# Optimization experiments

Hardware: AMD Instinct MI355X
Metric: run time of the kernel (lower is better)

## Reference

```python
import jax, jax.numpy as jnp
import numpy as np

N_NODES = 100000
N_EDGES = 300000
N_GRAPHS = 4096
EMB = 256
L = 5
EPS = 1e-5


def setup_inputs() -> dict:
    key = jax.random.key(0)
    ks = jax.random.split(key, 16)
    x = jax.random.normal(ks[0], (N_NODES, 40), dtype=jnp.float32)
    edge_index = jax.random.randint(ks[1], (2, N_EDGES), 0, N_NODES, dtype=jnp.int32)
    edge_attr = jax.random.normal(ks[2], (N_EDGES, 10), dtype=jnp.float32)
    batch = jnp.sort(jax.random.randint(ks[3], (N_NODES,), 0, N_GRAPHS, dtype=jnp.int32))
    s = lambda fan: 1.0 / np.sqrt(fan)
    params = {
        "x_emb_W": jax.random.normal(ks[4], (EMB, 40), jnp.float32) * np.sqrt(2.0 / 40),
        "x_emb_b": jnp.zeros((EMB,), jnp.float32),
        "e_emb_W": jax.random.normal(ks[5], (EMB, 10), jnp.float32) * np.sqrt(2.0 / 10),
        "e_emb_b": jnp.zeros((EMB,), jnp.float32),
        "gcn_W": jax.random.normal(ks[6], (L, EMB, EMB), jnp.float32) * s(EMB),
        "gcn_b": jax.random.normal(ks[7], (L, EMB), jnp.float32) * s(EMB),
        "root_emb": jax.random.normal(ks[8], (L, EMB), jnp.float32),
        "bn_gamma": jnp.ones((L, EMB), jnp.float32),
        "bn_beta": jnp.zeros((L, EMB), jnp.float32),
        "p1_W": jax.random.normal(ks[9], (EMB // 2, EMB), jnp.float32) * s(EMB),
        "p1_b": jnp.zeros((EMB // 2,), jnp.float32),
        "p2_W": jax.random.normal(ks[10], (EMB // 2, EMB // 2), jnp.float32) * s(EMB // 2),
        "p2_b": jnp.zeros((EMB // 2,), jnp.float32),
        "p3_W": jax.random.normal(ks[11], (1, EMB // 2), jnp.float32) * s(EMB // 2),
        "p3_b": jnp.zeros((1,), jnp.float32),
    }
    return dict(x=x, edge_index=edge_index, edge_attr=edge_attr, batch=batch, **params)


def _gcn_conv(h, row, col, ea, W, b, root):
    # h: [N, D] node feats; ea: [E, D] edge feats
    hx = h @ W.T + b
    deg = jax.ops.segment_sum(jnp.ones_like(row, dtype=hx.dtype), row, num_segments=N_NODES) + 1.0
    dinv = deg ** -0.5
    norm = dinv[row] * dinv[col]                      # [E]
    msg = norm[:, None] * jax.nn.relu(hx[row] + ea)   # gather + relu + scale
    agg = jax.ops.segment_sum(msg, col, num_segments=N_NODES)  # scatter-add to targets
    return agg + jax.nn.relu(hx + root) / deg[:, None]


def _batchnorm(h, gamma, beta):
    mean = jnp.mean(h, axis=0)
    var = jnp.var(h, axis=0)
    return (h - mean) * jax.lax.rsqrt(var + EPS) * gamma + beta


def reference(x, edge_index, edge_attr, batch,
              x_emb_W, x_emb_b, e_emb_W, e_emb_b,
              gcn_W, gcn_b, root_emb, bn_gamma, bn_beta,
              p1_W, p1_b, p2_W, p2_b, p3_W, p3_b):
    row, col = edge_index[0], edge_index[1]
    h = x @ x_emb_W.T + x_emb_b
    ea = edge_attr @ e_emb_W.T + e_emb_b
    for l in range(L):
        h_in = h
        h = _gcn_conv(h, row, col, ea, gcn_W[l], gcn_b[l], root_emb[l])
        h = _batchnorm(h_in + h, bn_gamma[l], bn_beta[l])
        if l != L - 1:
            h = jax.nn.relu(h)
        # dropout is identity in eval mode
    # global mean pool over graphs
    sums = jax.ops.segment_sum(h, batch, num_segments=N_GRAPHS)
    cnts = jax.ops.segment_sum(jnp.ones((h.shape[0],), h.dtype), batch, num_segments=N_GRAPHS)
    g = sums / jnp.maximum(cnts, 1.0)[:, None]
    # prediction head: Lin-ReLU-Lin-ReLU-Lin
    g = jax.nn.relu(g @ p1_W.T + p1_b)
    g = jax.nn.relu(g @ p2_W.T + p2_b)
    return g @ p3_W.T + p3_b
```

## Files before the change

kernel.cpp:

```cpp
#include <hip/hip_runtime.h>
#include <hip/hip_bf16.h>

#define NN 100000
#define NE 300000
#define NG 4096
#define EMB 256
#define NLAYERS 5

typedef unsigned short u16;
typedef unsigned int u32;

typedef short bf16x8 __attribute__((ext_vector_type(8)));
typedef float f32x4 __attribute__((ext_vector_type(4)));

__device__ __forceinline__ float b2f(u16 u){
    union { float f; u32 i; } v; v.i = ((u32)u) << 16; return v.f;
}
__device__ __forceinline__ u16 f2b(float f){
    __hip_bfloat16 h = __float2bfloat16(f);
    union { __hip_bfloat16 h; u16 u; } v; v.h = h; return v.u;
}

#define XNB 32
__global__ __launch_bounds__(256) void embed_x(const float* __restrict__ x,
        const float* __restrict__ W, const float* __restrict__ b,
        u16* __restrict__ t)
{
    __shared__ float sW[256][41];
    __shared__ float sx[XNB][40];
    int tid = threadIdx.x;
    for (int i = tid; i < 256*40; i += 256) sW[i/40][i%40] = W[i];
    int n0 = blockIdx.x * XNB;
    for (int i = tid; i < XNB*40; i += 256) {
        int j = i/40, k = i%40;
        sx[j][k] = x[(size_t)(n0+j)*40 + k];
    }
    __syncthreads();
    float bb = b[tid];
    for (int j = 0; j < XNB; ++j) {
        float a = bb;
        #pragma unroll
        for (int k = 0; k < 40; ++k) a = fmaf(sW[tid][k], sx[j][k], a);
        t[(size_t)(n0+j)*EMB + tid] = f2b(a);
    }
}

__global__ void wconv(const float* __restrict__ W, u16* __restrict__ Wb, int n)
{
    int i = blockIdx.x*256 + threadIdx.x;
    if (i < n) Wb[i] = f2b(W[i]);
}

__global__ void ewt_kernel(const float* __restrict__ eW, float* __restrict__ eWt)
{
    int i = blockIdx.x*256 + threadIdx.x;
    if (i < 2560) { int f = i/10, k = i%10; eWt[k*256 + f] = eW[i]; }
}

__global__ void hist_kernel(const int* __restrict__ row, const int* __restrict__ col,
        int* __restrict__ rcnt, int* __restrict__ ccnt, int E)
{
    int e = blockIdx.x*256 + threadIdx.x;
    if (e < E) {
        atomicAdd(&rcnt[row[e]], 1);
        atomicAdd(&ccnt[col[e]], 1);
    }
}

__global__ void deg_fin(const int* __restrict__ rcnt, float* __restrict__ dinv,
                        float* __restrict__ invdg, int N)
{
    int n = blockIdx.x*256 + threadIdx.x;
    if (n < N) {
        float d = (float)rcnt[n] + 1.0f;
        dinv[n]  = rsqrtf(d);
        invdg[n] = 1.0f/d;
    }
}

__global__ void scan1(const int* __restrict__ cnt, int* __restrict__ bsum, int N)
{
    __shared__ int sh[256];
    int t = threadIdx.x, i = blockIdx.x*256 + t;
    sh[t] = (i < N) ? cnt[i] : 0;
    __syncthreads();
    for (int off = 128; off > 0; off >>= 1) {
        if (t < off) sh[t] += sh[t+off];
        __syncthreads();
    }
    if (t == 0) bsum[blockIdx.x] = sh[0];
}

__global__ __launch_bounds__(512) void scan2(const int* __restrict__ bsum,
        int* __restrict__ bbase, int* __restrict__ coff, int nb)
{
    __shared__ int a[512], b[512];
    int t = threadIdx.x;
    a[t] = (t < nb) ? bsum[t] : 0;
    __syncthreads();
    int* src = a; int* dst = b;
    for (int off = 1; off < 512; off <<= 1) {
        dst[t] = (t >= off) ? src[t-off] + src[t] : src[t];
        __syncthreads();
        int* tmp = src; src = dst; dst = tmp;
    }
    bbase[t] = t ? src[t-1] : 0;
    if (t == 0) coff[NN] = NE;
}

__global__ void scan3(const int* __restrict__ cnt, const int* __restrict__ bbase,
        int* __restrict__ coff, int N)
{
    __shared__ int a[256], b[256];
    int t = threadIdx.x, i = blockIdx.x*256 + t;
    a[t] = (i < N) ? cnt[i] : 0;
    __syncthreads();
    int* src = a; int* dst = b;
    for (int off = 1; off < 256; off <<= 1) {
        dst[t] = (t >= off) ? src[t-off] + src[t] : src[t];
        __syncthreads();
        int* tmp = src; src = dst; dst = tmp;
    }
    if (i < N) coff[i] = bbase[blockIdx.x] + (t ? src[t-1] : 0);
}

__global__ void csr_fill(const int* __restrict__ row, const int* __restrict__ col,
        const float* __restrict__ eattr, const int* __restrict__ coff,
        const float* __restrict__ dinv, int* __restrict__ fill,
        int* __restrict__ erow, float* __restrict__ enorm,
        u16* __restrict__ eab, int E)
{
    int e = blockIdx.x*256 + threadIdx.x;
    if (e < E) {
        int c = col[e], r = row[e];
        int p = coff[c] + atomicAdd(&fill[c], 1);
        erow[p]  = r;
        enorm[p] = dinv[r] * dinv[c];
        #pragma unroll
        for (int k = 0; k < 10; ++k) eab[(size_t)p*16 + k] = f2b(eattr[(size_t)e*10 + k]);
        #pragma unroll
        for (int k = 10; k < 16; ++k) eab[(size_t)p*16 + k] = 0;
    }
}

__global__ __launch_bounds__(512) void gemm_mfma(const u16* __restrict__ A,
        const u16* __restrict__ Wb, const float* __restrict__ bias,
        const float* __restrict__ bnsc, int doBN,
        u16* __restrict__ C, int M)
{
    __shared__ u16 As[128*64];
    __shared__ u16 Bs[256*64];
    __shared__ float scS[256], shS[256];
    const int tid = threadIdx.x;
    if (doBN && tid < 256) { scS[tid] = bnsc[tid]; shS[tid] = bnsc[256+tid]; }
    const int wid  = tid >> 6;
    const int lane = tid & 63;
    const int wm = wid >> 2, wn = wid & 3;
    const int m0 = blockIdx.x * 128;
    __syncthreads();
    f32x4 acc[4][4] = {};
    for (int k0 = 0; k0 < 256; k0 += 64) {
        #pragma unroll
        for (int i = 0; i < 2; ++i) {
            int L = tid + i*512;
            int rowi = L >> 3, ch = L & 7;
            int sw = ch ^ (rowi & 7);
            int gr = m0 + rowi; gr = gr < M ? gr : M-1;
            uint4 va = *reinterpret_cast<const uint4*>(&A[(size_t)gr*256 + k0 + ch*8]);
            if (doBN) {
                int kk = k0 + ch*8;
                u32 wv[4] = {va.x, va.y, va.z, va.w};
                #pragma unroll
                for (int j = 0; j < 4; ++j) {
                    float lo = b2f((u16)(wv[j] & 0xffffu));
                    float hi = b2f((u16)(wv[j] >> 16));
                    lo = fmaxf(fmaf(lo, scS[kk+2*j],   shS[kk+2*j]),   0.f);
                    hi = fmaxf(fmaf(hi, scS[kk+2*j+1], shS[kk+2*j+1]), 0.f);
                    wv[j] = (u32)f2b(lo) | ((u32)f2b(hi) << 16);
                }
                va.x = wv[0]; va.y = wv[1]; va.z = wv[2]; va.w = wv[3];
            }
            *reinterpret_cast<uint4*>(&As[(rowi*8 + sw)*8]) = va;
        }
        #pragma unroll
        for (int i = 0; i < 4; ++i) {
            int L = tid + i*512;
            int rowi = L >> 3, ch = L & 7;
            int sw = ch ^ (rowi & 7);
            uint4 vb = *reinterpret_cast<const uint4*>(&Wb[(size_t)rowi*256 + k0 + ch*8]);
            *reinterpret_cast<uint4*>(&Bs[(rowi*8 + sw)*8]) = vb;
        }
        __syncthreads();
        const int c = lane >> 4;
        const int rl = lane & 15;
        #pragma unroll
        for (int kt = 0; kt < 2; ++kt) {
            bf16x8 af[4], bfr[4];
            #pragma unroll
            for (int f = 0; f < 4; ++f) {
                int ra = wm*64 + f*16 + rl;
                int cha = (kt*4 + c) ^ (ra & 7);
                af[f] = *reinterpret_cast<const bf16x8*>(&As[(ra*8 + cha)*8]);
                int rb = wn*64 + f*16 + rl;
                int chb = (kt*4 + c) ^ (rb & 7);
                bfr[f] = *reinterpret_cast<const bf16x8*>(&Bs[(rb*8 + chb)*8]);
            }
            #pragma unroll
            for (int fm = 0; fm < 4; ++fm)
                #pragma unroll
                for (int fn = 0; fn < 4; ++fn)
                    acc[fm][fn] = __builtin_amdgcn_mfma_f32_16x16x32_bf16(
                        af[fm], bfr[fn], acc[fm][fn], 0, 0, 0);
        }
        __syncthreads();
    }
    const int cn = lane & 15, rq = lane >> 4;
    #pragma unroll
    for (int fn = 0; fn < 4; ++fn) {
        int n = wn*64 + fn*16 + cn;
        float bb = bias[n];
        #pragma unroll
        for (int fm = 0; fm < 4; ++fm) {
            #pragma unroll
            for (int r = 0; r < 4; ++r) {
                int m = m0 + wm*64 + fm*16 + rq*4 + r;
                if (m < M) C[(size_t)m*256 + n] = f2b(acc[fm][fn][r] + bb);
            }
        }
    }
}

#define GFB 4
#define NGROUPS (NN/GFB)
__global__ __launch_bounds__(256) void gather_combine(const int* __restrict__ erow,
        const float* __restrict__ enorm, const u16* __restrict__ eab,
        const int* __restrict__ coff,
        const float* __restrict__ eWt, const float* __restrict__ ebv,
        const u16* __restrict__ hx, const float* __restrict__ rootv,
        const float* __restrict__ invdg, const float* __restrict__ bnscPrev,
        int doBN, u16* __restrict__ t, float* __restrict__ stats, int N)
{
    __shared__ float red[4][512];
    const int wid = threadIdx.x >> 6, lane = threadIdx.x & 63;
    const int f4 = lane*4;
    float w[4][10], bb[4];
    #pragma unroll
    for (int k = 0; k < 10; ++k) {
        float4 wv = *reinterpret_cast<const float4*>(&eWt[k*256 + f4]);
        w[0][k] = wv.x; w[1][k] = wv.y; w[2][k] = wv.z; w[3][k] = wv.w;
    }
    { float4 bv = *reinterpret_cast<const float4*>(&ebv[f4]);
      bb[0]=bv.x; bb[1]=bv.y; bb[2]=bv.z; bb[3]=bv.w; }
    float4 root = *reinterpret_cast<const float4*>(&rootv[f4]);
    float sc[4] = {1,1,1,1}, sh[4] = {0,0,0,0};
    if (doBN) {
        float4 s = *reinterpret_cast<const float4*>(&bnscPrev[f4]);
        float4 b = *reinterpret_cast<const float4*>(&bnscPrev[256+f4]);
        sc[0]=s.x; sc[1]=s.y; sc[2]=s.z; sc[3]=s.w;
        sh[0]=b.x; sh[1]=b.y; sh[2]=b.z; sh[3]=b.w;
    }
    float sacc[4] = {0,0,0,0}, s2acc[4] = {0,0,0,0};

    for (int g = blockIdx.x*4 + wid; g < NGROUPS; g += gridDim.x*4) {
        const int nb = g*GFB;
        int c1 = coff[nb+1], c2 = coff[nb+2], c3 = coff[nb+3], c4 = coff[nb+4];
        int s = coff[nb], e = c4;
        int jn = 0, cend = c1;
        float acc[4] = {0,0,0,0};

        #define FLUSH() do {                                                   \
            int n_ = nb + jn;                                                  \
            size_t idx_ = (size_t)n_*EMB + f4;                                 \
            uint2 hv_ = *reinterpret_cast<const uint2*>(&t[idx_]);             \
            uint2 xv_ = *reinterpret_cast<const uint2*>(&hx[idx_]);            \
            float id_ = invdg[n_];                                             \
            float hh_[4] = { b2f((u16)(hv_.x&0xffffu)), b2f((u16)(hv_.x>>16)), \
                             b2f((u16)(hv_.y&0xffffu)), b2f((u16)(hv_.y>>16)) };\
            float xx_[4] = { b2f((u16)(xv_.x&0xffffu)), b2f((u16)(xv_.x>>16)), \
                             b2f((u16)(xv_.y&0xffffu)), b2f((u16)(xv_.y>>16)) };\
            float rt_[4] = { root.x, root.y, root.z, root.w };                 \
            u16 ov_[4];                                                        \
            _Pragma("unroll")                                                  \
            for (int jj = 0; jj < 4; ++jj) {                                   \
                float hin_ = hh_[jj];                                          \
                if (doBN) hin_ = fmaxf(fmaf(hin_, sc[jj], sh[jj]), 0.f);       \
                float rv_ = xx_[jj] + rt_[jj];                                 \
                rv_ = rv_ > 0.f ? rv_ : 0.f;                                   \
                float tv_ = hin_ + acc[jj] + rv_*id_;                          \
                ov_[jj] = f2b(tv_);                                            \
                sacc[jj] += tv_; s2acc[jj] += tv_*tv_;                         \
                acc[jj] = 0.f;                                                 \
            }                                                                  \
            uint2 o_; o_.x = (u32)ov_[0] | ((u32)ov_[1]<<16);                  \
            o_.y = (u32)ov_[2] | ((u32)ov_[3]<<16);                            \
            *reinterpret_cast<uint2*>(&t[idx_]) = o_;                          \
            ++jn; cend = (jn==1) ? c2 : (jn==2) ? c3 : c4;                     \
        } while(0)

        #define CONSUME(nm, hvv, alo, ahi) do {                                \
            float hf_[4] = { b2f((u16)((hvv).x&0xffffu)), b2f((u16)((hvv).x>>16)),\
                             b2f((u16)((hvv).y&0xffffu)), b2f((u16)((hvv).y>>16)) };\
            float at_[10];                                                     \
            at_[0]=b2f((u16)((alo).x&0xffffu)); at_[1]=b2f((u16)((alo).x>>16));\
            at_[2]=b2f((u16)((alo).y&0xffffu)); at_[3]=b2f((u16)((alo).y>>16));\
            at_[4]=b2f((u16)((alo).z&0xffffu)); at_[5]=b2f((u16)((alo).z>>16));\
            at_[6]=b2f((u16)((alo).w&0xffffu)); at_[7]=b2f((u16)((alo).w>>16));\
            at_[8]=b2f((u16)((ahi).x&0xffffu)); at_[9]=b2f((u16)((ahi).x>>16));\
            _Pragma("unroll")                                                  \
            for (int jj = 0; jj < 4; ++jj) {                                   \
                float ea_ = bb[jj];                                            \
                _Pragma("unroll")                                              \
                for (int k = 0; k < 10; ++k) ea_ = fmaf(at_[k], w[jj][k], ea_);\
                float v_ = hf_[jj] + ea_;                                      \
                acc[jj] += v_ > 0.f ? v_*(nm) : 0.f;                           \
            }                                                                  \
        } while(0)

        int p = s;
        for (; p + 4 <= e; p += 4) {
            int r0 = erow[p], r1 = erow[p+1], r2 = erow[p+2], r3 = erow[p+3];
            float n0 = enorm[p], n1 = enorm[p+1], n2 = enorm[p+2], n3 = enorm[p+3];
            uint2 h0 = *reinterpret_cast<const uint2*>(&hx[(size_t)r0*EMB + f4]);
            uint2 h1 = *reinterpret_cast<const uint2*>(&hx[(size_t)r1*EMB + f4]);
            uint2 h2 = *reinterpret_cast<const uint2*>(&hx[(size_t)r2*EMB + f4]);
            uint2 h3 = *reinterpret_cast<const uint2*>(&hx[(size_t)r3*EMB + f4]);
            uint4 a0l = *reinterpret_cast<const uint4*>(&eab[(size_t)(p+0)*16]);
            uint4 a0h = *reinterpret_cast<const uint4*>(&eab[(size_t)(p+0)*16+8]);
            uint4 a1l = *reinterpret_cast<const uint4*>(&eab[(size_t)(p+1)*16]);
            uint4 a1h = *reinterpret_cast<const uint4*>(&eab[(size_t)(p+1)*16+8]);
            uint4 a2l = *reinterpret_cast<const uint4*>(&eab[(size_t)(p+2)*16]);
            uint4 a2h = *reinterpret_cast<const uint4*>(&eab[(size_t)(p+2)*16+8]);
            uint4 a3l = *reinterpret_cast<const uint4*>(&eab[(size_t)(p+3)*16]);
            uint4 a3h = *reinterpret_cast<const uint4*>(&eab[(size_t)(p+3)*16+8]);
            while (p+0 >= cend) FLUSH();
            CONSUME(n0, h0, a0l, a0h);
            while (p+1 >= cend) FLUSH();
            CONSUME(n1, h1, a1l, a1h);
            while (p+2 >= cend) FLUSH();
            CONSUME(n2, h2, a2l, a2h);
            while (p+3 >= cend) FLUSH();
            CONSUME(n3, h3, a3l, a3h);
        }
        for (; p < e; ++p) {
            int r0 = erow[p];
            float n0 = enorm[p];
            uint2 h0 = *reinterpret_cast<const uint2*>(&hx[(size_t)r0*EMB + f4]);
            uint4 a0l = *reinterpret_cast<const uint4*>(&eab[(size_t)p*16]);
            uint4 a0h = *reinterpret_cast<const uint4*>(&eab[(size_t)p*16+8]);
            while (p >= cend) FLUSH();
            CONSUME(n0, h0, a0l, a0h);
        }
        while (jn < GFB) FLUSH();
        #undef FLUSH
        #undef CONSUME
    }

    #pragma unroll
    for (int j = 0; j < 4; ++j) {
        red[wid][f4+j]     = sacc[j];
        red[wid][256+f4+j] = s2acc[j];
    }
    __syncthreads();
    int tt = threadIdx.x;
    float a0 = red[0][tt] + red[1][tt] + red[2][tt] + red[3][tt];
    float a1 = red[0][256+tt] + red[1][256+tt] + red[2][256+tt] + red[3][256+tt];
    atomicAdd(&stats[tt], a0);
    atomicAdd(&stats[256+tt], a1);
}

__global__ void bn_finalize(const float* __restrict__ stats,
        const float* __restrict__ gamma, const float* __restrict__ beta,
        float* __restrict__ sc, int N)
{
    int f = threadIdx.x;
    float inv = 1.0f / (float)N;
    float mean = stats[f] * inv;
    float var  = stats[256+f] * inv - mean*mean;
    float is = rsqrtf(var + 1e-5f);
    float scale = gamma[f] * is;
    sc[f] = scale;
    sc[256+f] = fmaf(-mean, scale, beta[f]);
}

__global__ __launch_bounds__(256) void pool_kernel(const u16* __restrict__ t,
        const int* __restrict__ batch, const float* __restrict__ bnsc4,
        float* __restrict__ psum, float* __restrict__ pcnt, int N)
{
    int tid = threadIdx.x;
    int half = tid >> 7;
    int pp = tid & 127;
    const u32* t32 = (const u32*)t;
    float sc0 = bnsc4[2*pp],     sc1 = bnsc4[2*pp+1];
    float sh0 = bnsc4[256+2*pp], sh1 = bnsc4[256+2*pp+1];
    int n0 = blockIdx.x * 256;
    int n1 = min(n0 + 256, N);
    int start = n0 + half;
    if (start >= n1) return;
    int cur = batch[start];
    float a0 = 0.f, a1 = 0.f;
    int cnt = 0;
    for (int n = start; n < n1; n += 2) {
        int gb = batch[n];
        if (gb != cur) {
            atomicAdd(&psum[(size_t)cur*EMB + 2*pp],   a0);
            atomicAdd(&psum[(size_t)cur*EMB + 2*pp+1], a1);
            if (pp == 0) atomicAdd(&pcnt[cur], (float)cnt);
            a0 = a1 = 0.f; cnt = 0; cur = gb;
        }
        u32 v = t32[(size_t)n*128 + pp];
        a0 += fmaf(b2f((u16)(v & 0xffffu)), sc0, sh0);
        a1 += fmaf(b2f((u16)(v >> 16)),     sc1, sh1);
        ++cnt;
    }
    atomicAdd(&psum[(size_t)cur*EMB + 2*pp],   a0);
    atomicAdd(&psum[(size_t)cur*EMB + 2*pp+1], a1);
    if (pp == 0) atomicAdd(&pcnt[cur], (float)cnt);
}

__global__ void pool2g(const float* __restrict__ psum, const float* __restrict__ pcnt,
        u16* __restrict__ gbf)
{
    int i = blockIdx.x*256 + threadIdx.x;
    if (i < NG*128) {
        int g = i >> 7, p2 = (i & 127)*2;
        float invc = 1.0f / fmaxf(pcnt[g], 1.0f);
        u32 pk = (u32)f2b(psum[(size_t)g*EMB + p2] * invc)
               | ((u32)f2b(psum[(size_t)g*EMB + p2 + 1] * invc) << 16);
        ((u32*)gbf)[i] = pk;
    }
}

__global__ __launch_bounds__(256) void gemm_head(const u16* __restrict__ A,
        const u16* __restrict__ W, const float* __restrict__ bias,
// ... 42 lines not shown
                        af[fm], bfr[fn], acc[fm][fn], 0, 0, 0);
        }
        __syncthreads();
    }
    const int cn = lane & 15, rq = lane >> 4;
    #pragma unroll
    for (int fn = 0; fn < 4; ++fn) {
        int n = wc*64 + fn*16 + cn;
        float bb = bias[n];
        #pragma unroll
        for (int fm = 0; fm < 4; ++fm) {
            #pragma unroll
            for (int r = 0; r < 4; ++r) {
                int m = m0 + wr*64 + fm*16 + rq*4 + r;
                if (m < M) C[(size_t)m*128 + n] = f2b(fmaxf(acc[fm][fn][r] + bb, 0.f));
            }
        }
    }
}

__global__ __launch_bounds__(256) void head_final(const u16* __restrict__ h2,
        const float* __restrict__ p3W, const float* __restrict__ p3b,
        float* __restrict__ out, int G)
{
    int tid = blockIdx.x*256 + threadIdx.x;
    int g = tid >> 4, sub = tid & 15;
    if (g >= G) return;
    uint4 v = *reinterpret_cast<const uint4*>(&h2[(size_t)g*128 + sub*8]);
    u32 wv[4] = {v.x, v.y, v.z, v.w};
    float s = 0.f;
    #pragma unroll
    for (int j = 0; j < 4; ++j) {
        s = fmaf(b2f((u16)(wv[j] & 0xffffu)), p3W[sub*8 + 2*j],   s);
        s = fmaf(b2f((u16)(wv[j] >> 16)),     p3W[sub*8 + 2*j+1], s);
    }
    s += __shfl_down(s, 8, 16);
    s += __shfl_down(s, 4, 16);
    s += __shfl_down(s, 2, 16);
    s += __shfl_down(s, 1, 16);
    if (sub == 0) out[g] = s + p3b[0];
}

extern "C" void kernel_launch(void* const* d_in, const int* in_sizes, int n_in,
                              void* d_out, int out_size, void* d_ws, size_t ws_size,
                              hipStream_t stream)
{
    const float* x     = (const float*)d_in[0];
    const int*   eidx  = (const int*)d_in[1];
    const float* eattr = (const float*)d_in[2];
    const int*   batch = (const int*)d_in[3];
    const float* xW    = (const float*)d_in[4];
    const float* xb    = (const float*)d_in[5];
    const float* eW    = (const float*)d_in[6];
    const float* eb    = (const float*)d_in[7];
    const float* gcnW  = (const float*)d_in[8];
    const float* gcnb  = (const float*)d_in[9];
    const float* rootE = (const float*)d_in[10];
    const float* bng   = (const float*)d_in[11];
    const float* bnb   = (const float*)d_in[12];
    const float* p1W   = (const float*)d_in[13];
    const float* p1b   = (const float*)d_in[14];
    const float* p2W   = (const float*)d_in[15];
    const float* p2b   = (const float*)d_in[16];
    const float* p3W   = (const float*)d_in[17];
    const float* p3b   = (const float*)d_in[18];
    float* out = (float*)d_out;

    const int* row = eidx;
    const int* col = eidx + NE;

    const size_t HSZ = (size_t)NN * EMB;
    const int NWB = 5*EMB*EMB;

    char* p = (char*)d_ws;
    u16* t   = (u16*)p;            p += HSZ*2;
    u16* hx  = (u16*)p;            p += HSZ*2;
    u16* Wb  = (u16*)p;            p += (size_t)NWB*2;
    float* eWt = (float*)p;        p += 2560*4;
    char* zbase = p;
    int* rcnt   = (int*)p;         p += (size_t)NN*4;
    int* ccnt   = (int*)p;         p += (size_t)NN*4;
    int* fill   = (int*)p;         p += (size_t)NN*4;
    float* stats= (float*)p;       p += (size_t)NLAYERS*512*4;
    float* psum = (float*)p;       p += (size_t)NG*EMB*4;
    float* pcnt = (float*)p;       p += (size_t)NG*4;
    size_t zbytes = (size_t)(p - zbase);
    float* dinv = (float*)p;       p += (size_t)NN*4;
    float* invdg= (float*)p;       p += (size_t)NN*4;
    float* bnscA= (float*)p;       p += (size_t)NLAYERS*512*4;
    int* coff   = (int*)p;         p += (size_t)(NN+1)*4;
    int* bsum   = (int*)p;         p += 512*4;
    int* bbase  = (int*)p;         p += 512*4;
    int* erow   = (int*)p;         p += (size_t)NE*4;
    float* enorm= (float*)p;       p += (size_t)NE*4;
    u16* eab    = (u16*)p;         p += (size_t)NE*16*2;
    u16* gbf    = (u16*)p;         p += (size_t)NG*EMB*2;
    u16* h1b    = (u16*)p;         p += (size_t)NG*128*2;
    u16* h2b    = (u16*)p;         p += (size_t)NG*128*2;
    u16* Wh1    = (u16*)p;         p += (size_t)128*256*2;
    u16* Wh2    = (u16*)p;         p += (size_t)128*128*2;
    size_t NEED = (size_t)(p - (char*)d_ws);
    if (ws_size < NEED) return;

    hipMemsetAsync(zbase, 0, zbytes, stream);

    const int NBS = (NN + 255)/256;

    embed_x<<<NN/XNB, 256, 0, stream>>>(x, xW, xb, t);
    wconv<<<(NWB+255)/256, 256, 0, stream>>>(gcnW, Wb, NWB);
    wconv<<<(128*256+255)/256, 256, 0, stream>>>(p1W, Wh1, 128*256);
    wconv<<<(128*128+255)/256, 256, 0, stream>>>(p2W, Wh2, 128*128);
    ewt_kernel<<<10, 256, 0, stream>>>(eW, eWt);
    hist_kernel<<<(NE+255)/256, 256, 0, stream>>>(row, col, rcnt, ccnt, NE);
    deg_fin<<<NBS, 256, 0, stream>>>(rcnt, dinv, invdg, NN);
    scan1<<<NBS, 256, 0, stream>>>(ccnt, bsum, NN);
    scan2<<<1, 512, 0, stream>>>(bsum, bbase, coff, NBS);
    scan3<<<NBS, 256, 0, stream>>>(ccnt, bbase, coff, NN);
    csr_fill<<<(NE+255)/256, 256, 0, stream>>>(row, col, eattr, coff, dinv, fill,
                                               erow, enorm, eab, NE);

    for (int l = 0; l < NLAYERS; ++l) {
        const u16*   Wl = Wb + (size_t)l*EMB*EMB;
        const float* bl = gcnb + (size_t)l*EMB;
        const float* rl = rootE + (size_t)l*EMB;
        const float* scPrev = bnscA + (size_t)(l > 0 ? l-1 : 0)*512;
        int doBN = (l > 0) ? 1 : 0;
        gemm_mfma<<<(NN+127)/128, 512, 0, stream>>>(t, Wl, bl, scPrev, doBN, hx, NN);
        gather_combine<<<1536, 256, 0, stream>>>(erow, enorm, eab, coff, eWt, eb,
                hx, rl, invdg, scPrev, doBN, t, stats + l*512, NN);
        bn_finalize<<<1, 256, 0, stream>>>(stats + l*512, bng + (size_t)l*EMB,
                                           bnb + (size_t)l*EMB, bnscA + (size_t)l*512, NN);
    }

    pool_kernel<<<NBS, 256, 0, stream>>>(t, batch, bnscA + (size_t)(NLAYERS-1)*512,
                                         psum, pcnt, NN);
    pool2g<<<(NG*128+255)/256, 256, 0, stream>>>(psum, pcnt, gbf);
    gemm_head<<<NG/128, 256, 0, stream>>>(gbf, Wh1, p1b, h1b, NG, 256);
    gemm_head<<<NG/128, 256, 0, stream>>>(h1b, Wh2, p2b, h2b, NG, 128);
    head_final<<<(NG*16+255)/256, 256, 0, stream>>>(h2b, p3W, p3b, out, NG);
}
```

Baseline: 970.1 us.

## Precompute full bf16 edge embeddings once and reuse across layers

When workspace allows, each edge's 256-wide embedding is computed once in bf16, in CSR order, by a new ea_kernel. The per-layer gather then streams these values with nontemporal loads instead of redoing the 10-term FMA for every edge, feature and layer. Row index and norm are packed into one int2 so each edge needs a single index load, and the gather grid grows to 2048 blocks. The trade is extra memory traffic (about 150MB of bf16 embeddings read in each layer) against the removed per-edge compute, with a fallback path kept for small workspaces.

Result: slower. 1.136 ms (+17.1%).

```diff
diff --git a/kernel.cpp b/kernel.cpp
--- a/kernel.cpp
+++ b/kernel.cpp
@@ -9,6 +9,7 @@
 
 typedef unsigned short u16;
 typedef unsigned int u32;
+typedef unsigned long long u64;
 
 typedef short bf16x8 __attribute__((ext_vector_type(8)));
 typedef float f32x4 __attribute__((ext_vector_type(4)));
@@ -127,19 +128,60 @@
 __global__ void csr_fill(const int* __restrict__ row, const int* __restrict__ col,
         const float* __restrict__ eattr, const int* __restrict__ coff,
         const float* __restrict__ dinv, int* __restrict__ fill,
-        int* __restrict__ erow, float* __restrict__ enorm,
-        u16* __restrict__ eab, int E)
+        int2* __restrict__ epack, int* __restrict__ eorig,
+        u16* __restrict__ eab, int modeA, int E)
 {
     int e = blockIdx.x*256 + threadIdx.x;
     if (e < E) {
         int c = col[e], r = row[e];
         int p = coff[c] + atomicAdd(&fill[c], 1);
-        erow[p]  = r;
-        enorm[p] = dinv[r] * dinv[c];
-        #pragma unroll
-        for (int k = 0; k < 10; ++k) eab[(size_t)p*16 + k] = f2b(eattr[(size_t)e*10 + k]);
-        #pragma unroll
-        for (int k = 10; k < 16; ++k) eab[(size_t)p*16 + k] = 0;
+        int2 ep; ep.x = r; ep.y = __float_as_int(dinv[r] * dinv[c]);
+        epack[p] = ep;
+        if (modeA) {
+            eorig[p] = e;
+        } else {
+            #pragma unroll
+            for (int k = 0; k < 10; ++k) eab[(size_t)p*16 + k] = f2b(eattr[(size_t)e*10 + k]);
+            #pragma unroll
+            for (int k = 10; k < 16; ++k) eab[(size_t)p*16 + k] = 0;
+        }
+    }
+}
+
+__global__ __launch_bounds__(256) void ea_kernel(const int* __restrict__ eorig,
+        const float* __restrict__ eattr, const float* __restrict__ eWt,
+        const float* __restrict__ ebv, u16* __restrict__ ea, int E)
+{
+    const int wid = threadIdx.x >> 6, lane = threadIdx.x & 63;
+    const int f4 = lane*4;
+    float w[4][10], bb[4];
+    #pragma unroll
+    for (int k = 0; k < 10; ++k) {
+        float4 wv = *reinterpret_cast<const float4*>(&eWt[k*256 + f4]);
+        w[0][k] = wv.x; w[1][k] = wv.y; w[2][k] = wv.z; w[3][k] = wv.w;
+    }
+    { float4 bv = *reinterpret_cast<const float4*>(&ebv[f4]);
+      bb[0]=bv.x; bb[1]=bv.y; bb[2]=bv.z; bb[3]=bv.w; }
+    int p0 = (blockIdx.x*4 + wid)*4;
+    #pragma unroll
+    for (int j = 0; j < 4; ++j) {
+        int p = p0 + j;
+        if (p < E) {
+            int e = eorig[p];
+            float at[10];
+            #pragma unroll
+            for (int k = 0; k < 10; ++k) at[k] = eattr[(size_t)e*10 + k];
+            u16 o[4];
+            #pragma unroll
+            for (int jj = 0; jj < 4; ++jj) {
+                float v = bb[jj];
+                #pragma unroll
+                for (int k = 0; k < 10; ++k) v = fmaf(at[k], w[jj][k], v);
+                o[jj] = f2b(v);
+            }
+            uint2 ov; ov.x = (u32)o[0] | ((u32)o[1]<<16); ov.y = (u32)o[2] | ((u32)o[3]<<16);
+            *reinterpret_cast<uint2*>(&ea[(size_t)p*256 + f4]) = ov;
+        }
     }
 }
 
@@ -232,10 +274,8 @@
 
 #define GFB 4
 #define NGROUPS (NN/GFB)
-__global__ __launch_bounds__(256) void gather_combine(const int* __restrict__ erow,
-        const float* __restrict__ enorm, const u16* __restrict__ eab,
-        const int* __restrict__ coff,
-        const float* __restrict__ eWt, const float* __restrict__ ebv,
+__global__ __launch_bounds__(256) void gather_combine_ea(const int2* __restrict__ epack,
+        const u16* __restrict__ ea, const int* __restrict__ coff,
         const u16* __restrict__ hx, const float* __restrict__ rootv,
         const float* __restrict__ invdg, const float* __restrict__ bnscPrev,
         int doBN, u16* __restrict__ t, float* __restrict__ stats, int N)
@@ -243,14 +283,6 @@
     __shared__ float red[4][512];
     const int wid = threadIdx.x >> 6, lane = threadIdx.x & 63;
     const int f4 = lane*4;
-    float w[4][10], bb[4];
-    #pragma unroll
-    for (int k = 0; k < 10; ++k) {
-        float4 wv = *reinterpret_cast<const float4*>(&eWt[k*256 + f4]);
-        w[0][k] = wv.x; w[1][k] = wv.y; w[2][k] = wv.z; w[3][k] = wv.w;
-    }
-    { float4 bv = *reinterpret_cast<const float4*>(&ebv[f4]);
-      bb[0]=bv.x; bb[1]=bv.y; bb[2]=bv.z; bb[3]=bv.w; }
     float4 root = *reinterpret_cast<const float4*>(&rootv[f4]);
     float sc[4] = {1,1,1,1}, sh[4] = {0,0,0,0};
     if (doBN) {
@@ -297,6 +329,127 @@
             ++jn; cend = (jn==1) ? c2 : (jn==2) ? c3 : c4;                     \
         } while(0)
 
+        #define CONSUME(nm, hvv, ev) do {                                      \
+            float hf_[4] = { b2f((u16)((hvv).x&0xffffu)), b2f((u16)((hvv).x>>16)),\
+                             b2f((u16)((hvv).y&0xffffu)), b2f((u16)((hvv).y>>16)) };\
+            float ef_[4] = { b2f((u16)((ev)&0xffffu)),       b2f((u16)(((ev)>>16)&0xffffu)),\
+                             b2f((u16)(((ev)>>32)&0xffffu)), b2f((u16)((ev)>>48)) };\
+            _Pragma("unroll")                                                  \
+            for (int jj = 0; jj < 4; ++jj) {                                   \
+                float v_ = hf_[jj] + ef_[jj];                                  \
+                acc[jj] += v_ > 0.f ? v_*(nm) : 0.f;                           \
+            }                                                                  \
+        } while(0)
+
+        int p = s;
+        for (; p + 4 <= e; p += 4) {
+            int2 e0 = epack[p], e1 = epack[p+1], e2 = epack[p+2], e3 = epack[p+3];
+            uint2 h0 = *reinterpret_cast<const uint2*>(&hx[(size_t)e0.x*EMB + f4]);
+            uint2 h1 = *reinterpret_cast<const uint2*>(&hx[(size_t)e1.x*EMB + f4]);
+            uint2 h2 = *reinterpret_cast<const uint2*>(&hx[(size_t)e2.x*EMB + f4]);
+            uint2 h3 = *reinterpret_cast<const uint2*>(&hx[(size_t)e3.x*EMB + f4]);
+            u64 v0 = __builtin_nontemporal_load((const u64*)&ea[(size_t)(p+0)*256 + f4]);
+            u64 v1 = __builtin_nontemporal_load((const u64*)&ea[(size_t)(p+1)*256 + f4]);
+            u64 v2 = __builtin_nontemporal_load((const u64*)&ea[(size_t)(p+2)*256 + f4]);
+            u64 v3 = __builtin_nontemporal_load((const u64*)&ea[(size_t)(p+3)*256 + f4]);
+            while (p+0 >= cend) FLUSH();
+            CONSUME(__int_as_float(e0.y), h0, v0);
+            while (p+1 >= cend) FLUSH();
+            CONSUME(__int_as_float(e1.y), h1, v1);
+            while (p+2 >= cend) FLUSH();
+            CONSUME(__int_as_float(e2.y), h2, v2);
+            while (p+3 >= cend) FLUSH();
+            CONSUME(__int_as_float(e3.y), h3, v3);
+        }
+        for (; p < e; ++p) {
+            int2 e0 = epack[p];
+            uint2 h0 = *reinterpret_cast<const uint2*>(&hx[(size_t)e0.x*EMB + f4]);
+            u64 v0 = __builtin_nontemporal_load((const u64*)&ea[(size_t)p*256 + f4]);
+            while (p >= cend) FLUSH();
+            CONSUME(__int_as_float(e0.y), h0, v0);
+        }
+        while (jn < GFB) FLUSH();
+        #undef FLUSH
+        #undef CONSUME
+    }
+
+    #pragma unroll
+    for (int j = 0; j < 4; ++j) {
+        red[wid][f4+j]     = sacc[j];
+        red[wid][256+f4+j] = s2acc[j];
+    }
+    __syncthreads();
+    int tt = threadIdx.x;
+    float a0 = red[0][tt] + red[1][tt] + red[2][tt] + red[3][tt];
+    float a1 = red[0][256+tt] + red[1][256+tt] + red[2][256+tt] + red[3][256+tt];
+    atomicAdd(&stats[tt], a0);
+    atomicAdd(&stats[256+tt], a1);
+}
+
+__global__ __launch_bounds__(256) void gather_combine_w(const int2* __restrict__ epack,
+        const u16* __restrict__ eab, const int* __restrict__ coff,
+        const float* __restrict__ eWt, const float* __restrict__ ebv,
+        const u16* __restrict__ hx, const float* __restrict__ rootv,
+        const float* __restrict__ invdg, const float* __restrict__ bnscPrev,
+        int doBN, u16* __restrict__ t, float* __restrict__ stats, int N)
+{
+    __shared__ float red[4][512];
+    const int wid = threadIdx.x >> 6, lane = threadIdx.x & 63;
+    const int f4 = lane*4;
+    float w[4][10], bb[4];
+    #pragma unroll
+    for (int k = 0; k < 10; ++k) {
+        float4 wv = *reinterpret_cast<const float4*>(&eWt[k*256 + f4]);
+        w[0][k] = wv.x; w[1][k] = wv.y; w[2][k] = wv.z; w[3][k] = wv.w;
+    }
+    { float4 bv = *reinterpret_cast<const float4*>(&ebv[f4]);
+      bb[0]=bv.x; bb[1]=bv.y; bb[2]=bv.z; bb[3]=bv.w; }
+    float4 root = *reinterpret_cast<const float4*>(&rootv[f4]);
+    float sc[4] = {1,1,1,1}, sh[4] = {0,0,0,0};
+    if (doBN) {
+        float4 s = *reinterpret_cast<const float4*>(&bnscPrev[f4]);
+        float4 b = *reinterpret_cast<const float4*>(&bnscPrev[256+f4]);
+        sc[0]=s.x; sc[1]=s.y; sc[2]=s.z; sc[3]=s.w;
+        sh[0]=b.x; sh[1]=b.y; sh[2]=b.z; sh[3]=b.w;
+    }
+    float sacc[4] = {0,0,0,0}, s2acc[4] = {0,0,0,0};
+
+    for (int g = blockIdx.x*4 + wid; g < NGROUPS; g += gridDim.x*4) {
+        const int nb = g*GFB;
+        int c1 = coff[nb+1], c2 = coff[nb+2], c3 = coff[nb+3], c4 = coff[nb+4];
+        int s = coff[nb], e = c4;
+        int jn = 0, cend = c1;
+        float acc[4] = {0,0,0,0};
+
+        #define FLUSH() do {                                                   \
+            int n_ = nb + jn;                                                  \
+            size_t idx_ = (size_t)n_*EMB + f4;                                 \
+            uint2 hv_ = *reinterpret_cast<const uint2*>(&t[idx_]);             \
+            uint2 xv_ = *reinterpret_cast<const uint2*>(&hx[idx_]);            \
+            float id_ = invdg[n_];                                             \
+            float hh_[4] = { b2f((u16)(hv_.x&0xffffu)), b2f((u16)(hv_.x>>16)), \
+                             b2f((u16)(hv_.y&0xffffu)), b2f((u16)(hv_.y>>16)) };\
+            float xx_[4] = { b2f((u16)(xv_.x&0xffffu)), b2f((u16)(xv_.x>>16)), \
+                             b2f((u16)(xv_.y&0xffffu)), b2f((u16)(xv_.y>>16)) };\
+            float rt_[4] = { root.x, root.y, root.z, root.w };                 \
+            u16 ov_[4];                                                        \
+            _Pragma("unroll")                                                  \
+            for (int jj = 0; jj < 4; ++jj) {                                   \
+                float hin_ = hh_[jj];                                          \
+                if (doBN) hin_ = fmaxf(fmaf(hin_, sc[jj], sh[jj]), 0.f);       \
+                float rv_ = xx_[jj] + rt_[jj];                                 \
+                rv_ = rv_ > 0.f ? rv_ : 0.f;                                   \
+                float tv_ = hin_ + acc[jj] + rv_*id_;                          \
+                ov_[jj] = f2b(tv_);                                            \
+                sacc[jj] += tv_; s2acc[jj] += tv_*tv_;                         \
+                acc[jj] = 0.f;                                                 \
+            }                                                                  \
+            uint2 o_; o_.x = (u32)ov_[0] | ((u32)ov_[1]<<16);                  \
+            o_.y = (u32)ov_[2] | ((u32)ov_[3]<<16);                            \
+            *reinterpret_cast<uint2*>(&t[idx_]) = o_;                          \
+            ++jn; cend = (jn==1) ? c2 : (jn==2) ? c3 : c4;                     \
+        } while(0)
+
         #define CONSUME(nm, hvv, alo, ahi) do {                                \
             float hf_[4] = { b2f((u16)((hvv).x&0xffffu)), b2f((u16)((hvv).x>>16)),\
                              b2f((u16)((hvv).y&0xffffu)), b2f((u16)((hvv).y>>16)) };\
@@ -318,12 +471,11 @@
 
         int p = s;
         for (; p + 4 <= e; p += 4) {
-            int r0 = erow[p], r1 = erow[p+1], r2 = erow[p+2], r3 = erow[p+3];
-            float n0 = enorm[p], n1 = enorm[p+1], n2 = enorm[p+2], n3 = enorm[p+3];
-            uint2 h0 = *reinterpret_cast<const uint2*>(&hx[(size_t)r0*EMB + f4]);
-            uint2 h1 = *reinterpret_cast<const uint2*>(&hx[(size_t)r1*EMB + f4]);
-            uint2 h2 = *reinterpret_cast<const uint2*>(&hx[(size_t)r2*EMB + f4]);
-            uint2 h3 = *reinterpret_cast<const uint2*>(&hx[(size_t)r3*EMB + f4]);
+            int2 e0 = epack[p], e1 = epack[p+1], e2 = epack[p+2], e3 = epack[p+3];
+            uint2 h0 = *reinterpret_cast<const uint2*>(&hx[(size_t)e0.x*EMB + f4]);
+            uint2 h1 = *reinterpret_cast<const uint2*>(&hx[(size_t)e1.x*EMB + f4]);
+            uint2 h2 = *reinterpret_cast<const uint2*>(&hx[(size_t)e2.x*EMB + f4]);
+            uint2 h3 = *reinterpret_cast<const uint2*>(&hx[(size_t)e3.x*EMB + f4]);
             uint4 a0l = *reinterpret_cast<const uint4*>(&eab[(size_t)(p+0)*16]);
             uint4 a0h = *reinterpret_cast<const uint4*>(&eab[(size_t)(p+0)*16+8]);
             uint4 a1l = *reinterpret_cast<const uint4*>(&eab[(size_t)(p+1)*16]);
@@ -333,22 +485,21 @@
             uint4 a3l = *reinterpret_cast<const uint4*>(&eab[(size_t)(p+3)*16]);
             uint4 a3h = *reinterpret_cast<const uint4*>(&eab[(size_t)(p+3)*16+8]);
             while (p+0 >= cend) FLUSH();
-            CONSUME(n0, h0, a0l, a0h);
+            CONSUME(__int_as_float(e0.y), h0, a0l, a0h);
             while (p+1 >= cend) FLUSH();
-            CONSUME(n1, h1, a1l, a1h);
+            CONSUME(__int_as_float(e1.y), h1, a1l, a1h);
             while (p+2 >= cend) FLUSH();
-            CONSUME(n2, h2, a2l, a2h);
+            CONSUME(__int_as_float(e2.y), h2, a2l, a2h);
             while (p+3 >= cend) FLUSH();
-            CONSUME(n3, h3, a3l, a3h);
+            CONSUME(__int_as_float(e3.y), h3, a3l, a3h);
         }
         for (; p < e; ++p) {
-            int r0 = erow[p];
-            float n0 = enorm[p];
-            uint2 h0 = *reinterpret_cast<const uint2*>(&hx[(size_t)r0*EMB + f4]);
+            int2 e0 = epack[p];
+            uint2 h0 = *reinterpret_cast<const uint2*>(&hx[(size_t)e0.x*EMB + f4]);
             uint4 a0l = *reinterpret_cast<const uint4*>(&eab[(size_t)p*16]);
             uint4 a0h = *reinterpret_cast<const uint4*>(&eab[(size_t)p*16+8]);
             while (p >= cend) FLUSH();
-            CONSUME(n0, h0, a0l, a0h);
+            CONSUME(__int_as_float(e0.y), h0, a0l, a0h);
         }
         while (jn < GFB) FLUSH();
         #undef FLUSH
@@ -557,8 +708,6 @@
     int* ccnt   = (int*)p;         p += (size_t)NN*4;
     int* fill   = (int*)p;         p += (size_t)NN*4;
     float* stats= (float*)p;       p += (size_t)NLAYERS*512*4;
-    float* psum = (float*)p;       p += (size_t)NG*EMB*4;
-    float* pcnt = (float*)p;       p += (size_t)NG*4;
     size_t zbytes = (size_t)(p - zbase);
     float* dinv = (float*)p;       p += (size_t)NN*4;
     float* invdg= (float*)p;       p += (size_t)NN*4;
@@ -566,16 +715,31 @@
     int* coff   = (int*)p;         p += (size_t)(NN+1)*4;
     int* bsum   = (int*)p;         p += 512*4;
     int* bbase  = (int*)p;         p += 512*4;
-    int* erow   = (int*)p;         p += (size_t)NE*4;
-    float* enorm= (float*)p;       p += (size_t)NE*4;
-    u16* eab    = (u16*)p;         p += (size_t)NE*16*2;
-    u16* gbf    = (u16*)p;         p += (size_t)NG*EMB*2;
-    u16* h1b    = (u16*)p;         p += (size_t)NG*128*2;
-    u16* h2b    = (u16*)p;         p += (size_t)NG*128*2;
-    u16* Wh1    = (u16*)p;         p += (size_t)128*256*2;
-    u16* Wh2    = (u16*)p;         p += (size_t)128*128*2;
-    size_t NEED = (size_t)(p - (char*)d_ws);
-    if (ws_size < NEED) return;
+    int2* epack = (int2*)p;        p += (size_t)NE*8;
+    int* eorig  = (int*)p;         p += (size_t)NE*4;
+    char* tail  = p;
+
+    const size_t EA_BYTES   = HSZ ? (size_t)NE*EMB*2 : 0;
+    const size_t EAB_BYTES  = (size_t)NE*16*2;
+    const size_t HEAD_BYTES = (size_t)NG*EMB*4 + NG*4
+                            + (size_t)NG*EMB*2
+                            + (size_t)NG*128*2*2
+                            + (size_t)(128*256 + 128*128)*2;
+    const size_t NEED_A = (size_t)(tail - (char*)d_ws) + EA_BYTES;
+    const size_t NEED_B = (size_t)(tail - (char*)d_ws) + EAB_BYTES + HEAD_BYTES;
+    int modeA = (ws_size >= NEED_A) ? 1 : 0;
+    if (!modeA && ws_size < NEED_B) return;
+
+    u16* ea  = (u16*)tail;
+    u16* eab = (u16*)tail;
+    char* hb = modeA ? tail : (tail + EAB_BYTES);
+    float* psum = (float*)hb;      hb += (size_t)NG*EMB*4;
+    float* pcnt = (float*)hb;      hb += (size_t)NG*4;
+    u16* gbf    = (u16*)hb;        hb += (size_t)NG*EMB*2;
+    u16* h1b    = (u16*)hb;        hb += (size_t)NG*128*2;
+    u16* h2b    = (u16*)hb;        hb += (size_t)NG*128*2;
+    u16* Wh1    = (u16*)hb;        hb += (size_t)128*256*2;
+    u16* Wh2    = (u16*)hb;        hb += (size_t)128*128*2;
 
     hipMemsetAsync(zbase, 0, zbytes, stream);
 
@@ -583,8 +747,6 @@
 
     embed_x<<<NN/XNB, 256, 0, stream>>>(x, xW, xb, t);
     wconv<<<(NWB+255)/256, 256, 0, stream>>>(gcnW, Wb, NWB);
-    wconv<<<(128*256+255)/256, 256, 0, stream>>>(p1W, Wh1, 128*256);
-    wconv<<<(128*128+255)/256, 256, 0, stream>>>(p2W, Wh2, 128*128);
     ewt_kernel<<<10, 256, 0, stream>>>(eW, eWt);
     hist_kernel<<<(NE+255)/256, 256, 0, stream>>>(row, col, rcnt, ccnt, NE);
     deg_fin<<<NBS, 256, 0, stream>>>(rcnt, dinv, invdg, NN);
@@ -592,7 +754,9 @@
     scan2<<<1, 512, 0, stream>>>(bsum, bbase, coff, NBS);
     scan3<<<NBS, 256, 0, stream>>>(ccnt, bbase, coff, NN);
     csr_fill<<<(NE+255)/256, 256, 0, stream>>>(row, col, eattr, coff, dinv, fill,
-                                               erow, enorm, eab, NE);
+                                               epack, eorig, eab, modeA, NE);
+    if (modeA)
+        ea_kernel<<<(NE+15)/16, 256, 0, stream>>>(eorig, eattr, eWt, eb, ea, NE);
 
     for (int l = 0; l < NLAYERS; ++l) {
         const u16*   Wl = Wb + (size_t)l*EMB*EMB;
@@ -601,11 +765,19 @@
         const float* scPrev = bnscA + (size_t)(l > 0 ? l-1 : 0)*512;
         int doBN = (l > 0) ? 1 : 0;
         gemm_mfma<<<(NN+127)/128, 512, 0, stream>>>(t, Wl, bl, scPrev, doBN, hx, NN);
-        gather_combine<<<1536, 256, 0, stream>>>(erow, enorm, eab, coff, eWt, eb,
-                hx, rl, invdg, scPrev, doBN, t, stats + l*512, NN);
+        if (modeA)
+            gather_combine_ea<<<2048, 256, 0, stream>>>(epack, ea, coff, hx, rl,
+                    invdg, scPrev, doBN, t, stats + l*512, NN);
+        else
+            gather_combine_w<<<2048, 256, 0, stream>>>(epack, eab, coff, eWt, eb,
+                    hx, rl, invdg, scPrev, doBN, t, stats + l*512, NN);
         bn_finalize<<<1, 256, 0, stream>>>(stats + l*512, bng + (size_t)l*EMB,
                                            bnb + (size_t)l*EMB, bnscA + (size_t)l*512, NN);
     }
+
+    hipMemsetAsync(psum, 0, (size_t)NG*EMB*4 + NG*4, stream);
+    wconv<<<(128*256+255)/256, 256, 0, stream>>>(p1W, Wh1, 128*256);
+    wconv<<<(128*128+255)/256, 256, 0, stream>>>(p2W, Wh2, 128*128);
 
     pool_kernel<<<NBS, 256, 0, stream>>>(t, batch, bnscA + (size_t)(NLAYERS-1)*512,
                                          psum, pcnt, NN);
```

## Prefetch GEMM tiles into registers, stage output via LDS, pack edge row/norm

Applied to the files above, without the earlier changes.

The GEMM now loads the next K-slice of A and W into registers while the MFMAs for the current slice run, so global latency overlaps compute. Its epilogue stages bf16 results through shared memory and writes them as coalesced 16-byte stores instead of scattered 2-byte stores. Edge source index and normalisation are packed into one int2 array so the gather does one load per edge instead of two. The gather grid grows from 1536 to 2048 blocks. The register prefetch raises register pressure, and the epilogue adds two extra barriers per pass.

Result: slower. 991.6 us (+2.2%).

```diff
diff --git a/kernel.cpp b/kernel.cpp
--- a/kernel.cpp
+++ b/kernel.cpp
@@ -9,6 +9,7 @@
 
 typedef unsigned short u16;
 typedef unsigned int u32;
+typedef unsigned long long u64;
 
 typedef short bf16x8 __attribute__((ext_vector_type(8)));
 typedef float f32x4 __attribute__((ext_vector_type(4)));
@@ -127,15 +128,14 @@
 __global__ void csr_fill(const int* __restrict__ row, const int* __restrict__ col,
         const float* __restrict__ eattr, const int* __restrict__ coff,
         const float* __restrict__ dinv, int* __restrict__ fill,
-        int* __restrict__ erow, float* __restrict__ enorm,
-        u16* __restrict__ eab, int E)
+        int2* __restrict__ epack, u16* __restrict__ eab, int E)
 {
     int e = blockIdx.x*256 + threadIdx.x;
     if (e < E) {
         int c = col[e], r = row[e];
         int p = coff[c] + atomicAdd(&fill[c], 1);
-        erow[p]  = r;
-        enorm[p] = dinv[r] * dinv[c];
+        int2 ep; ep.x = r; ep.y = __float_as_int(dinv[r] * dinv[c]);
+        epack[p] = ep;
         #pragma unroll
         for (int k = 0; k < 10; ++k) eab[(size_t)p*16 + k] = f2b(eattr[(size_t)e*10 + k]);
         #pragma unroll
@@ -143,54 +143,70 @@
     }
 }
 
+#define CS_STRIDE 144
 __global__ __launch_bounds__(512) void gemm_mfma(const u16* __restrict__ A,
         const u16* __restrict__ Wb, const float* __restrict__ bias,
         const float* __restrict__ bnsc, int doBN,
         u16* __restrict__ C, int M)
 {
-    __shared__ u16 As[128*64];
-    __shared__ u16 Bs[256*64];
-    __shared__ float scS[256], shS[256];
+    __shared__ __align__(16) char smem[51200];
+    u16* As = (u16*)smem;
+    u16* Bs = (u16*)(smem + 16384);
+    float* scS = (float*)(smem + 49152);
+    float* shS = scS + 256;
     const int tid = threadIdx.x;
     if (doBN && tid < 256) { scS[tid] = bnsc[tid]; shS[tid] = bnsc[256+tid]; }
     const int wid  = tid >> 6;
     const int lane = tid & 63;
     const int wm = wid >> 2, wn = wid & 3;
     const int m0 = blockIdx.x * 128;
-    __syncthreads();
+    const int r8 = tid >> 3;
+    const int ch = tid & 7;
+    const int sw = ch ^ (r8 & 7);
+    const int ga0 = min(m0 + r8,      M-1);
+    const int ga1 = min(m0 + r8 + 64, M-1);
+
+    uint4 ra[2], rb[4];
+    #define LOADK(k0) do {                                                     \
+        ra[0] = *reinterpret_cast<const uint4*>(&A[(size_t)ga0*256 + (k0) + ch*8]); \
+        ra[1] = *reinterpret_cast<const uint4*>(&A[(size_t)ga1*256 + (k0) + ch*8]); \
+        rb[0] = *reinterpret_cast<const uint4*>(&Wb[(size_t)(r8+  0)*256 + (k0) + ch*8]); \
+        rb[1] = *reinterpret_cast<const uint4*>(&Wb[(size_t)(r8+ 64)*256 + (k0) + ch*8]); \
+        rb[2] = *reinterpret_cast<const uint4*>(&Wb[(size_t)(r8+128)*256 + (k0) + ch*8]); \
+        rb[3] = *reinterpret_cast<const uint4*>(&Wb[(size_t)(r8+192)*256 + (k0) + ch*8]); \
+    } while(0)
+
+    LOADK(0);
+    if (doBN) __syncthreads();
     f32x4 acc[4][4] = {};
     for (int k0 = 0; k0 < 256; k0 += 64) {
-        #pragma unroll
-        for (int i = 0; i < 2; ++i) {
-            int L = tid + i*512;
-            int rowi = L >> 3, ch = L & 7;
-            int sw = ch ^ (rowi & 7);
-            int gr = m0 + rowi; gr = gr < M ? gr : M-1;
-            uint4 va = *reinterpret_cast<const uint4*>(&A[(size_t)gr*256 + k0 + ch*8]);
-            if (doBN) {
-                int kk = k0 + ch*8;
-                u32 wv[4] = {va.x, va.y, va.z, va.w};
-                #pragma unroll
-                for (int j = 0; j < 4; ++j) {
-                    float lo = b2f((u16)(wv[j] & 0xffffu));
-                    float hi = b2f((u16)(wv[j] >> 16));
-                    lo = fmaxf(fmaf(lo, scS[kk+2*j],   shS[kk+2*j]),   0.f);
-                    hi = fmaxf(fmaf(hi, scS[kk+2*j+1], shS[kk+2*j+1]), 0.f);
-                    wv[j] = (u32)f2b(lo) | ((u32)f2b(hi) << 16);
-                }
-                va.x = wv[0]; va.y = wv[1]; va.z = wv[2]; va.w = wv[3];
+        uint4 va0 = ra[0], va1 = ra[1];
+        if (doBN) {
+            int kk = k0 + ch*8;
+            u32 w0[4] = {va0.x, va0.y, va0.z, va0.w};
+            u32 w1[4] = {va1.x, va1.y, va1.z, va1.w};
+            #pragma unroll
+            for (int j = 0; j < 4; ++j) {
+                float l0 = b2f((u16)(w0[j] & 0xffffu)), h0 = b2f((u16)(w0[j] >> 16));
+                float l1 = b2f((u16)(w1[j] & 0xffffu)), h1 = b2f((u16)(w1[j] >> 16));
+                float s0 = scS[kk+2*j], s1 = scS[kk+2*j+1];
+                float b0 = shS[kk+2*j], b1 = shS[kk+2*j+1];
+                l0 = fmaxf(fmaf(l0, s0, b0), 0.f); h0 = fmaxf(fmaf(h0, s1, b1), 0.f);
+                l1 = fmaxf(fmaf(l1, s0, b0), 0.f); h1 = fmaxf(fmaf(h1, s1, b1), 0.f);
+                w0[j] = (u32)f2b(l0) | ((u32)f2b(h0) << 16);
+                w1[j] = (u32)f2b(l1) | ((u32)f2b(h1) << 16);
             }
-            *reinterpret_cast<uint4*>(&As[(rowi*8 + sw)*8]) = va;
-        }
-        #pragma unroll
-        for (int i = 0; i < 4; ++i) {
-            int L = tid + i*512;
-            int rowi = L >> 3, ch = L & 7;
-            int sw = ch ^ (rowi & 7);
-            uint4 vb = *reinterpret_cast<const uint4*>(&Wb[(size_t)rowi*256 + k0 + ch*8]);
-            *reinterpret_cast<uint4*>(&Bs[(rowi*8 + sw)*8]) = vb;
-        }
-        __syncthreads();
+            va0.x=w0[0]; va0.y=w0[1]; va0.z=w0[2]; va0.w=w0[3];
+            va1.x=w1[0]; va1.y=w1[1]; va1.z=w1[2]; va1.w=w1[3];
+        }
+        *reinterpret_cast<uint4*>(&As[((r8     )*8 + sw)*8]) = va0;
+        *reinterpret_cast<uint4*>(&As[((r8 + 64)*8 + sw)*8]) = va1;
+        *reinterpret_cast<uint4*>(&Bs[((r8     )*8 + sw)*8]) = rb[0];
+        *reinterpret_cast<uint4*>(&Bs[((r8+ 64 )*8 + sw)*8]) = rb[1];
+        *reinterpret_cast<uint4*>(&Bs[((r8+128 )*8 + sw)*8]) = rb[2];
+        *reinterpret_cast<uint4*>(&Bs[((r8+192 )*8 + sw)*8]) = rb[3];
+        __syncthreads();
+        if (k0 < 192) LOADK(k0 + 64);
         const int c = lane >> 4;
         const int rl = lane & 15;
         #pragma unroll
@@ -198,12 +214,12 @@
             bf16x8 af[4], bfr[4];
             #pragma unroll
             for (int f = 0; f < 4; ++f) {
-                int ra = wm*64 + f*16 + rl;
-                int cha = (kt*4 + c) ^ (ra & 7);
-                af[f] = *reinterpret_cast<const bf16x8*>(&As[(ra*8 + cha)*8]);
-                int rb = wn*64 + f*16 + rl;
-                int chb = (kt*4 + c) ^ (rb & 7);
-                bfr[f] = *reinterpret_cast<const bf16x8*>(&Bs[(rb*8 + chb)*8]);
+                int rA = wm*64 + f*16 + rl;
+                int cha = (kt*4 + c) ^ (rA & 7);
+                af[f] = *reinterpret_cast<const bf16x8*>(&As[(rA*8 + cha)*8]);
+                int rB = wn*64 + f*16 + rl;
+                int chb = (kt*4 + c) ^ (rB & 7);
+                bfr[f] = *reinterpret_cast<const bf16x8*>(&Bs[(rB*8 + chb)*8]);
             }
             #pragma unroll
             for (int fm = 0; fm < 4; ++fm)
@@ -214,27 +230,47 @@
         }
         __syncthreads();
     }
+    #undef LOADK
+
+    u16* Cs = (u16*)smem;
     const int cn = lane & 15, rq = lane >> 4;
     #pragma unroll
-    for (int fn = 0; fn < 4; ++fn) {
-        int n = wn*64 + fn*16 + cn;
-        float bb = bias[n];
-        #pragma unroll
-        for (int fm = 0; fm < 4; ++fm) {
+    for (int pp = 0; pp < 2; ++pp) {
+        if ((wn >> 1) == pp) {
+            int cl0 = (wn & 1)*64;
             #pragma unroll
-            for (int r = 0; r < 4; ++r) {
-                int m = m0 + wm*64 + fm*16 + rq*4 + r;
-                if (m < M) C[(size_t)m*256 + n] = f2b(acc[fm][fn][r] + bb);
+            for (int fn = 0; fn < 4; ++fn) {
+                int n = wn*64 + fn*16 + cn;
+                float bb = bias[n];
+                #pragma unroll
+                for (int fm = 0; fm < 4; ++fm) {
+                    int rbase = wm*64 + fm*16 + rq*4;
+                    #pragma unroll
+                    for (int r = 0; r < 4; ++r)
+                        Cs[(rbase + r)*CS_STRIDE + cl0 + fn*16 + cn] =
+                            f2b(acc[fm][fn][r] + bb);
+                }
             }
         }
+        __syncthreads();
+        #pragma unroll
+        for (int it = 0; it < 4; ++it) {
+            int idx = tid + it*512;
+            int rowi = idx >> 4;
+            int c8  = (idx & 15) * 8;
+            int m = m0 + rowi;
+            if (m < M)
+                *reinterpret_cast<uint4*>(&C[(size_t)m*256 + pp*128 + c8]) =
+                    *reinterpret_cast<const uint4*>(&Cs[rowi*CS_STRIDE + c8]);
+        }
+        __syncthreads();
     }
 }
 
 #define GFB 4
 #define NGROUPS (NN/GFB)
-__global__ __launch_bounds__(256) void gather_combine(const int* __restrict__ erow,
-        const float* __restrict__ enorm, const u16* __restrict__ eab,
-        const int* __restrict__ coff,
+__global__ __launch_bounds__(256) void gather_combine_w(const int2* __restrict__ epack,
+        const u16* __restrict__ eab, const int* __restrict__ coff,
         const float* __restrict__ eWt, const float* __restrict__ ebv,
         const u16* __restrict__ hx, const float* __restrict__ rootv,
         const float* __restrict__ invdg, const float* __restrict__ bnscPrev,
@@ -318,12 +354,11 @@
 
         int p = s;
         for (; p + 4 <= e; p += 4) {
-            int r0 = erow[p], r1 = erow[p+1], r2 = erow[p+2], r3 = erow[p+3];
-            float n0 = enorm[p], n1 = enorm[p+1], n2 = enorm[p+2], n3 = enorm[p+3];
-            uint2 h0 = *reinterpret_cast<const uint2*>(&hx[(size_t)r0*EMB + f4]);
-            uint2 h1 = *reinterpret_cast<const uint2*>(&hx[(size_t)r1*EMB + f4]);
-            uint2 h2 = *reinterpret_cast<const uint2*>(&hx[(size_t)r2*EMB + f4]);
-            uint2 h3 = *reinterpret_cast<const uint2*>(&hx[(size_t)r3*EMB + f4]);
+            int2 e0 = epack[p], e1 = epack[p+1], e2 = epack[p+2], e3 = epack[p+3];
+            uint2 h0 = *reinterpret_cast<const uint2*>(&hx[(size_t)e0.x*EMB + f4]);
+            uint2 h1 = *reinterpret_cast<const uint2*>(&hx[(size_t)e1.x*EMB + f4]);
+            uint2 h2 = *reinterpret_cast<const uint2*>(&hx[(size_t)e2.x*EMB + f4]);
+            uint2 h3 = *reinterpret_cast<const uint2*>(&hx[(size_t)e3.x*EMB + f4]);
             uint4 a0l = *reinterpret_cast<const uint4*>(&eab[(size_t)(p+0)*16]);
             uint4 a0h = *reinterpret_cast<const uint4*>(&eab[(size_t)(p+0)*16+8]);
             uint4 a1l = *reinterpret_cast<const uint4*>(&eab[(size_t)(p+1)*16]);
@@ -333,22 +368,21 @@
             uint4 a3l = *reinterpret_cast<const uint4*>(&eab[(size_t)(p+3)*16]);
             uint4 a3h = *reinterpret_cast<const uint4*>(&eab[(size_t)(p+3)*16+8]);
             while (p+0 >= cend) FLUSH();
-            CONSUME(n0, h0, a0l, a0h);
+            CONSUME(__int_as_float(e0.y), h0, a0l, a0h);
             while (p+1 >= cend) FLUSH();
-            CONSUME(n1, h1, a1l, a1h);
+            CONSUME(__int_as_float(e1.y), h1, a1l, a1h);
             while (p+2 >= cend) FLUSH();
-            CONSUME(n2, h2, a2l, a2h);
+            CONSUME(__int_as_float(e2.y), h2, a2l, a2h);
             while (p+3 >= cend) FLUSH();
-            CONSUME(n3, h3, a3l, a3h);
+            CONSUME(__int_as_float(e3.y), h3, a3l, a3h);
         }
         for (; p < e; ++p) {
-            int r0 = erow[p];
-            float n0 = enorm[p];
-            uint2 h0 = *reinterpret_cast<const uint2*>(&hx[(size_t)r0*EMB + f4]);
+            int2 e0 = epack[p];
+            uint2 h0 = *reinterpret_cast<const uint2*>(&hx[(size_t)e0.x*EMB + f4]);
             uint4 a0l = *reinterpret_cast<const uint4*>(&eab[(size_t)p*16]);
             uint4 a0h = *reinterpret_cast<const uint4*>(&eab[(size_t)p*16+8]);
             while (p >= cend) FLUSH();
-            CONSUME(n0, h0, a0l, a0h);
+            CONSUME(__int_as_float(e0.y), h0, a0l, a0h);
         }
         while (jn < GFB) FLUSH();
         #undef FLUSH
@@ -566,8 +600,7 @@
     int* coff   = (int*)p;         p += (size_t)(NN+1)*4;
     int* bsum   = (int*)p;         p += 512*4;
     int* bbase  = (int*)p;         p += 512*4;
-    int* erow   = (int*)p;         p += (size_t)NE*4;
-    float* enorm= (float*)p;       p += (size_t)NE*4;
+    int2* epack = (int2*)p;        p += (size_t)NE*8;
     u16* eab    = (u16*)p;         p += (size_t)NE*16*2;
     u16* gbf    = (u16*)p;         p += (size_t)NG*EMB*2;
     u16* h1b    = (u16*)p;         p += (size_t)NG*128*2;
@@ -592,7 +625,7 @@
     scan2<<<1, 512, 0, stream>>>(bsum, bbase, coff, NBS);
     scan3<<<NBS, 256, 0, stream>>>(ccnt, bbase, coff, NN);
     csr_fill<<<(NE+255)/256, 256, 0, stream>>>(row, col, eattr, coff, dinv, fill,
-                                               erow, enorm, eab, NE);
+                                               epack, eab, NE);
 
     for (int l = 0; l < NLAYERS; ++l) {
         const u16*   Wl = Wb + (size_t)l*EMB*EMB;
@@ -601,7 +634,7 @@
         const float* scPrev = bnscA + (size_t)(l > 0 ? l-1 : 0)*512;
         int doBN = (l > 0) ? 1 : 0;
         gemm_mfma<<<(NN+127)/128, 512, 0, stream>>>(t, Wl, bl, scPrev, doBN, hx, NN);
-        gather_combine<<<1536, 256, 0, stream>>>(erow, enorm, eab, coff, eWt, eb,
+        gather_combine_w<<<2048, 256, 0, stream>>>(epack, eab, coff, eWt, eb,
                 hx, rl, invdg, scPrev, doBN, t, stats + l*512, NN);
         bn_finalize<<<1, 256, 0, stream>>>(stats + l*512, bng + (size_t)l*EMB,
                                            bnb + (size_t)l*EMB, bnscA + (size_t)l*512, NN);
```
